# Kernel tuning notes

Hardware: AMD Instinct MI355X
Metric: run time of the kernel (lower is better)

The kernel has to match this reference:

```python
import jax, jax.numpy as jnp
import numpy as np

N_NODES = 100000
N_EDGES = 1600000
F_IN, F_HID, F_OUT = 128, 128, 16
NEG_SLOPE = 0.2


def _glorot(key, shape):
    fan = sum(shape)
    return jax.random.uniform(key, shape, jnp.float32, -1.0, 1.0) * jnp.sqrt(6.0 / fan)


def setup_inputs() -> dict:
    key = jax.random.key(0)
    ks = jax.random.split(key, 16)
    x = jax.random.normal(ks[0], (N_NODES, F_IN), jnp.float32)
    edge_index = jax.random.randint(ks[1], (2, N_EDGES), 0, N_NODES, jnp.int64)
    d1, d2, d3 = F_HID, F_HID // 2, F_OUT
    return {
        'x': x,
        'edge_index': edge_index,
        'W1': _glorot(ks[2], (F_IN, d1)), 'a_src1': _glorot(ks[3], (d1,)), 'a_dst1': _glorot(ks[4], (d1,)), 'b1': jnp.zeros((d1,), jnp.float32),
        'W2': _glorot(ks[5], (d1, d2)), 'a_src2': _glorot(ks[6], (d2,)), 'a_dst2': _glorot(ks[7], (d2,)), 'b2': jnp.zeros((d2,), jnp.float32),
        'W3': _glorot(ks[8], (d2, d3)), 'a_src3': _glorot(ks[9], (d3,)), 'a_dst3': _glorot(ks[10], (d3,)), 'b3': jnp.zeros((d3,), jnp.float32),
    }


def gat_conv(x, src, dst, W, a_s, a_d, b):
    # x: [N, Fin] -> h: [N, Fout]; src/dst: [E] (self-loops included)
    h = x @ W
    e = jax.nn.leaky_relu(h @ a_s, NEG_SLOPE * 0 + NEG_SLOPE)  # placeholder avoided below
    # attention logits per edge: leaky_relu(alpha_src[src] + alpha_dst[dst])
    al_s = h @ a_s  # [N]
    al_d = h @ a_d  # [N]
    logits = jax.nn.leaky_relu(al_s[src] + al_d[dst], NEG_SLOPE)  # [E]
    # numerically stable softmax over incoming edges of each dst node
    m = jax.ops.segment_max(logits, dst, num_segments=N_NODES)
    m = jnp.where(jnp.isfinite(m), m, 0.0)
    ex = jnp.exp(logits - m[dst])
    denom = jax.ops.segment_sum(ex, dst, num_segments=N_NODES)
    alpha = ex / denom[dst]  # self-loops guarantee denom > 0
    out = jax.ops.segment_sum(alpha[:, None] * h[src], dst, num_segments=N_NODES)
    return out + b


def reference(x, edge_index, W1, a_src1, a_dst1, b1, W2, a_src2, a_dst2, b2, W3, a_src3, a_dst3, b3):
    loops = jnp.arange(N_NODES, dtype=edge_index.dtype)
    src = jnp.concatenate([edge_index[0], loops])
    dst = jnp.concatenate([edge_index[1], loops])
    h = gat_conv(x, src, dst, W1, a_src1, a_dst1, b1)
    h = jax.nn.relu(h)  # dropout p=0.5 is identity in eval mode
    h = gat_conv(h, src, dst, W2, a_src2, a_dst2, b2)
    h = jax.nn.relu(h)
    out = gat_conv(h, src, dst, W3, a_src3, a_dst3, b3)
    return out
```

## Files before the change

### kernel.cpp

```cpp
#include <hip/hip_runtime.h>
#include <hip/hip_bf16.h>

typedef __hip_bfloat16 bf16;
typedef __attribute__((ext_vector_type(8))) __bf16 bf16x8;
typedef __attribute__((ext_vector_type(4))) float f32x4;

static constexpr int N = 100000;
static constexpr int E = 1600000;
static constexpr int ETOT = E + N;
static constexpr float SLOPE = 0.2f;

__device__ __constant__ int c_poff[12] = {0, 16384, 16512, 16640,
                                          16768, 24960, 25024, 25088,
                                          25152, 26176, 26192, 26208};
static constexpr int PTOT = 26224;
static constexpr int H_POFF[12] = {0, 16384, 16512, 16640, 16768, 24960,
                                   25024, 25088, 25152, 26176, 26192, 26208};

struct Src12 { const void* p[12]; };

__device__ __forceinline__ float bfLo(unsigned u) { return __uint_as_float(u << 16); }
__device__ __forceinline__ float bfHi(unsigned u) { return __uint_as_float(u & 0xFFFF0000u); }

__device__ __forceinline__ void fma8(const uint4 r, float e, float* acc) {
  acc[0] = fmaf(e, bfLo(r.x), acc[0]);
  acc[1] = fmaf(e, bfHi(r.x), acc[1]);
  acc[2] = fmaf(e, bfLo(r.y), acc[2]);
  acc[3] = fmaf(e, bfHi(r.y), acc[3]);
  acc[4] = fmaf(e, bfLo(r.z), acc[4]);
  acc[5] = fmaf(e, bfHi(r.z), acc[5]);
  acc[6] = fmaf(e, bfLo(r.w), acc[6]);
  acc[7] = fmaf(e, bfHi(r.w), acc[7]);
}

__device__ __forceinline__ float edge_ex(float l) {
  l = (l > 0.f) ? l : SLOPE * l;
  return __expf(l);
}

__device__ __forceinline__ void loadEdge(const int* __restrict__ ei32,
                                         const long long* __restrict__ ei64,
                                         int use64, int t, int& s, int& d) {
  if (t >= E) { s = d = t - E; return; }
  if (use64) { s = (int)ei64[t]; d = (int)ei64[E + t]; }
  else       { s = ei32[t];      d = ei32[E + t]; }
}

static constexpr int NSCAN = (N + 255) / 256;

__global__ __launch_bounds__(256) void detect_zero_kernel(
    const unsigned long long* __restrict__ ei64,
    const unsigned short* __restrict__ w1u16,
    int* __restrict__ flags, int* __restrict__ cnt) {
  const int t = threadIdx.x;
  const int i = blockIdx.x * 256 + t;
  if (i < N) cnt[i] = 0;
  if (blockIdx.x == 0) {
    __shared__ unsigned long long bl[4];
    __shared__ unsigned long long sb64;
    const int w = t >> 6;
    bool p64 = (t < 64) && (ei64[t] >= (unsigned long long)N);
    unsigned long long b64 = __ballot(p64);
    if (t == 0) sb64 = b64;
    bool pf = (((w1u16[t] >> 7) & 0xFFu) >= 126u);
    unsigned long long bf_ = __ballot(pf);
    if ((t & 63) == 0) bl[w] = bf_;
    __syncthreads();
    if (t == 0) {
      flags[0] = (sb64 == 0ull) ? 1 : 0;
      flags[1] = ((bl[0] | bl[1] | bl[2] | bl[3]) != 0ull) ? 1 : 0;
    }
  }
}

static constexpr int PB_DEG = (ETOT + 255) / 256;
static constexpr int PB_X   = N * 128 / 4 / 256;
static constexpr int PB_PAR = (PTOT + 255) / 256;
static constexpr int PB_W1  = 128 * 128 / 256;
static constexpr int PB_W2  = 128 * 64 / 256;
static constexpr int PB_W3  = 64 * 16 / 256;
static constexpr int PB_TOT = PB_DEG + PB_X + PB_PAR + PB_W1 + PB_W2 + PB_W3;

__device__ __forceinline__ void conv_w(const void* W, int kd, int dout, int f32,
                                       bf16* __restrict__ wt, int idx) {
  int n = idx / kd, k = idx - n * kd;
  float v = f32 ? ((const float*)W)[k * dout + n]
                : __bfloat162float(((const bf16*)W)[k * dout + n]);
  wt[idx] = __float2bfloat16(v);
}

__global__ __launch_bounds__(256) void prep_kernel(
    const int* __restrict__ ei32, const long long* __restrict__ ei64,
    const int* __restrict__ flags, int* __restrict__ cnt, int* __restrict__ rank,
    const void* __restrict__ x, bf16* __restrict__ xb,
    Src12 s, float* __restrict__ prm,
    bf16* __restrict__ w1t, bf16* __restrict__ w2t, bf16* __restrict__ w3t) {
  const int b = blockIdx.x, tid = threadIdx.x;
  const int f64 = flags[0], f32 = flags[1];
  if (b < PB_DEG) {
    int t = b * 256 + tid;
    if (t < ETOT) {
      int d = (t >= E) ? (t - E) : (f64 ? (int)ei64[E + t] : ei32[E + t]);
      rank[t] = atomicAdd(&cnt[d], 1);
    }
  } else if (b < PB_DEG + PB_X) {
    int t = (b - PB_DEG) * 256 + tid;
    if (f32) {
      float4 v = ((const float4*)x)[t];
      xb[4 * t + 0] = __float2bfloat16(v.x);
      xb[4 * t + 1] = __float2bfloat16(v.y);
      xb[4 * t + 2] = __float2bfloat16(v.z);
      xb[4 * t + 3] = __float2bfloat16(v.w);
    } else {
      ((uint2*)xb)[t] = ((const uint2*)x)[t];
    }
  } else if (b < PB_DEG + PB_X + PB_PAR) {
    int t = (b - PB_DEG - PB_X) * 256 + tid;
    if (t < PTOT) {
      int k = 0;
#pragma unroll
      for (int i = 1; i < 12; ++i)
        if (t >= c_poff[i]) k = i;
      int j = t - c_poff[k];
      prm[t] = f32 ? ((const float*)s.p[k])[j]
                   : __bfloat162float(((const bf16*)s.p[k])[j]);
    }
  } else if (b < PB_DEG + PB_X + PB_PAR + PB_W1) {
    conv_w(s.p[0], 128, 128, f32, w1t, (b - PB_DEG - PB_X - PB_PAR) * 256 + tid);
  } else if (b < PB_DEG + PB_X + PB_PAR + PB_W1 + PB_W2) {
    conv_w(s.p[4], 128, 64, f32, w2t, (b - PB_DEG - PB_X - PB_PAR - PB_W1) * 256 + tid);
  } else {
    conv_w(s.p[8], 64, 16, f32, w3t, (b - PB_DEG - PB_X - PB_PAR - PB_W1 - PB_W2) * 256 + tid);
  }
}

__global__ __launch_bounds__(256) void scan1_kernel(const int* __restrict__ cnt,
                                                    int* __restrict__ bsum) {
  __shared__ int red[256];
  const int t = threadIdx.x;
  const int i = blockIdx.x * 256 + t;
  red[t] = (i < N) ? cnt[i] : 0;
  __syncthreads();
#pragma unroll
  for (int off = 128; off > 0; off >>= 1) {
    if (t < off) red[t] += red[t + off];
    __syncthreads();
  }
  if (t == 0) bsum[blockIdx.x] = red[0];
}

__global__ __launch_bounds__(1024) void scan2_kernel(const int* __restrict__ bsum,
                                                     int* __restrict__ boff) {
  __shared__ int s[1024];
  const int t = threadIdx.x;
  const int v = (t < NSCAN) ? bsum[t] : 0;
  s[t] = v;
  __syncthreads();
  for (int off = 1; off < 1024; off <<= 1) {
    int u = (t >= off) ? s[t - off] : 0;
    __syncthreads();
    s[t] += u;
    __syncthreads();
  }
  if (t < NSCAN) boff[t] = s[t] - v;
}

__global__ __launch_bounds__(256) void scan3_kernel(const int* __restrict__ cnt,
                                                    const int* __restrict__ boff,
                                                    int* __restrict__ rowptr) {
  __shared__ int s[256];
  const int t = threadIdx.x;
  const int i = blockIdx.x * 256 + t;
  const int v = (i < N) ? cnt[i] : 0;
  s[t] = v;
  __syncthreads();
#pragma unroll
  for (int off = 1; off < 256; off <<= 1) {
    int u = (t >= off) ? s[t - off] : 0;
    __syncthreads();
    s[t] += u;
    __syncthreads();
  }
  if (i < N) rowptr[i] = boff[blockIdx.x] + s[t] - v;
  if (i == 0) rowptr[N] = ETOT;
}

template <int KD, int DOUT>
__device__ __forceinline__ void gemm_body(int bb, const unsigned short* __restrict__ inb,
                                          const unsigned short* __restrict__ wt,
                                          bf16* __restrict__ h,
                                          const float* __restrict__ a_s,
                                          const float* __restrict__ a_d,
                                          float* __restrict__ als,
                                          float* __restrict__ ald) {
  constexpr int SA = KD + 8;
  constexpr int NT = DOUT / 16;
  constexpr int KS = KD / 32;
  __shared__ unsigned short sA[64 * SA];
  __shared__ unsigned short sB[DOUT * SA];
  const int tid = threadIdx.x;
  const int m0 = bb * 64;
  for (int idx = tid; idx < DOUT * KD / 8; idx += 256) {
    int n = idx / (KD / 8), k8 = idx - n * (KD / 8);
    *(uint4*)(sB + n * SA + k8 * 8) = *(const uint4*)(wt + n * KD + k8 * 8);
  }
  for (int idx = tid; idx < 64 * KD / 8; idx += 256) {
    int r = idx / (KD / 8), k8 = idx - r * (KD / 8);
    int m = m0 + r;
    uint4 v = make_uint4(0, 0, 0, 0);
    if (m < N) v = *(const uint4*)(inb + (size_t)m * KD + k8 * 8);
    *(uint4*)(sA + r * SA + k8 * 8) = v;
  }
  __syncthreads();
  const int lane = tid & 63;
  const int wv = tid >> 6;
  const int lr = lane & 15;
  const int q = lane >> 4;
  f32x4 acc[NT];
#pragma unroll
  for (int t = 0; t < NT; ++t)
#pragma unroll
    for (int r = 0; r < 4; ++r) acc[t][r] = 0.f;
  const int arow = wv * 16 + lr;
#pragma unroll
  for (int ks = 0; ks < KS; ++ks) {
    const int k0 = ks * 32 + q * 8;
    const bf16x8 a = *(const bf16x8*)(sA + arow * SA + k0);
#pragma unroll
    for (int t = 0; t < NT; ++t) {
      const bf16x8 b = *(const bf16x8*)(sB + (t * 16 + lr) * SA + k0);
      acc[t] = __builtin_amdgcn_mfma_f32_16x16x32_bf16(a, b, acc[t], 0, 0, 0);
    }
  }
  float ps[4] = {0.f, 0.f, 0.f, 0.f}, pd[4] = {0.f, 0.f, 0.f, 0.f};
#pragma unroll
  for (int t = 0; t < NT; ++t) {
    const float av = a_s[t * 16 + lr];
    const float dv = a_d[t * 16 + lr];
#pragma unroll
    for (int r = 0; r < 4; ++r) {
      ps[r] = fmaf(acc[t][r], av, ps[r]);
      pd[r] = fmaf(acc[t][r], dv, pd[r]);
    }
  }
#pragma unroll
  for (int m = 1; m < 16; m <<= 1)
#pragma unroll
    for (int r = 0; r < 4; ++r) {
      ps[r] += __shfl_xor(ps[r], m, 64);
      pd[r] += __shfl_xor(pd[r], m, 64);
    }
  const int mb = m0 + wv * 16 + q * 4;
  if (lr == 0) {
#pragma unroll
    for (int r = 0; r < 4; ++r) {
      int m = mb + r;
      if (m < N) { als[m] = ps[r]; ald[m] = pd[r]; }
    }
  }
#pragma unroll
  for (int t = 0; t < NT; ++t)
#pragma unroll
    for (int r = 0; r < 4; ++r) {
      int m = mb + r;
      if (m < N) h[(size_t)m * DOUT + t * 16 + lr] = __float2bfloat16(acc[t][r]);
    }
}

template <int KD, int DOUT>
__global__ __launch_bounds__(256) void gemm_al(const unsigned short* __restrict__ inb,
                                               const unsigned short* __restrict__ wt,
                                               bf16* __restrict__ h,
                                               const float* __restrict__ a_s,
                                               const float* __restrict__ a_d,
                                               float* __restrict__ als,
                                               float* __restrict__ ald) {
  gemm_body<KD, DOUT>(blockIdx.x, inb, wt, h, a_s, a_d, als, ald);
}

static constexpr int GB1 = (N + 63) / 64;

__global__ __launch_bounds__(256) void gemm1_scatter(
    const unsigned short* __restrict__ inb, const unsigned short* __restrict__ wt,
    bf16* __restrict__ h, const float* __restrict__ a_s, const float* __restrict__ a_d,
    float* __restrict__ als, float* __restrict__ ald,
    const int* __restrict__ ei32, const long long* __restrict__ ei64,
    const int* __restrict__ flags, const int* __restrict__ rank,
    const int* __restrict__ rowptr, int* __restrict__ ssrt) {
  if (blockIdx.x < GB1) {
    gemm_body<128, 128>(blockIdx.x, inb, wt, h, a_s, a_d, als, ald);
  } else {
    int t = (blockIdx.x - GB1) * 256 + threadIdx.x;
    if (t < ETOT) {
      int s, d;
      loadEdge(ei32, ei64, flags[0], t, s, d);
      ssrt[rowptr[d] + rank[t]] = s;
    }
  }
}

template <int DOUT, bool RELU, bool FINAL>
__global__ __launch_bounds__(256) void aggregate_csr(const int* __restrict__ rowptr,
                                                     const int* __restrict__ ssrt,
                                                     const float* __restrict__ als,
                                                     const float* __restrict__ ald,
                                                     const unsigned short* __restrict__ hb,
                                                     const float* __restrict__ bias,
                                                     bf16* __restrict__ outb,
                                                     void* __restrict__ outv,
                                                     const int* __restrict__ flags) {
  constexpr int TPN = DOUT / 8;
  constexpr int NPB = 256 / TPN;
  const int sub = threadIdx.x % TPN;
  const int d = blockIdx.x * NPB + threadIdx.x / TPN;
  if (d >= N) return;
  const int p0 = rowptr[d], p1 = rowptr[d + 1];
  const float ad = ald[d];
  const int col0 = sub * 8;
  float acc[8];
#pragma unroll
  for (int c = 0; c < 8; ++c) acc[c] = 0.f;
  float sum = 0.f;
  int p = p0;
  for (; p + 4 <= p1; p += 4) {
    const int s0 = ssrt[p + 0];
    const int s1 = ssrt[p + 1];
    const int s2 = ssrt[p + 2];
    const int s3 = ssrt[p + 3];
    const uint4 r0 = *reinterpret_cast<const uint4*>(hb + (size_t)s0 * DOUT + col0);
    const uint4 r1 = *reinterpret_cast<const uint4*>(hb + (size_t)s1 * DOUT + col0);
    const uint4 r2 = *reinterpret_cast<const uint4*>(hb + (size_t)s2 * DOUT + col0);
    const uint4 r3 = *reinterpret_cast<const uint4*>(hb + (size_t)s3 * DOUT + col0);
    const float x0 = edge_ex(als[s0] + ad);
    const float x1 = edge_ex(als[s1] + ad);
    const float x2 = edge_ex(als[s2] + ad);
    const float x3 = edge_ex(als[s3] + ad);
    sum += (x0 + x1) + (x2 + x3);
    fma8(r0, x0, acc);
    fma8(r1, x1, acc);
    fma8(r2, x2, acc);
    fma8(r3, x3, acc);
  }
  for (; p < p1; ++p) {
    const int s = ssrt[p];
    const uint4 r = *reinterpret_cast<const uint4*>(hb + (size_t)s * DOUT + col0);
    const float x = edge_ex(als[s] + ad);
    sum += x;
    fma8(r, x, acc);
  }
  const float inv = 1.f / sum;
  if (FINAL) {
    const bool f32o = flags[1] != 0;
#pragma unroll
    for (int c = 0; c < 8; ++c) {
      float v = acc[c] * inv + bias[col0 + c];
      if (f32o) ((float*)outv)[(size_t)d * DOUT + col0 + c] = v;
      else      ((bf16*)outv)[(size_t)d * DOUT + col0 + c] = __float2bfloat16(v);
    }
  } else {
#pragma unroll
    for (int c = 0; c < 8; ++c) {
      float v = acc[c] * inv + bias[col0 + c];
      if (RELU) v = (v > 0.f) ? v : 0.f;
      outb[(size_t)d * DOUT + col0 + c] = __float2bfloat16(v);
    }
  }
}

static inline size_t rup(size_t v) { return (v + 255) & ~(size_t)255; }

extern "C" void kernel_launch(void* const* d_in, const int* in_sizes, int n_in,
                              void* d_out, int out_size, void* d_ws, size_t ws_size,
                              hipStream_t stream) {
  const int* ei32 = (const int*)d_in[1];
  const long long* ei64 = (const long long*)d_in[1];

  char* p = (char*)d_ws;
  int*   flags  = (int*)p;   p += 256;
  float* prm    = (float*)p; p += rup((size_t)PTOT * 4);
  bf16*  w1t    = (bf16*)p;  p += rup((size_t)128 * 128 * 2);
  bf16*  w2t    = (bf16*)p;  p += rup((size_t)128 * 64 * 2);
  bf16*  w3t    = (bf16*)p;  p += rup((size_t)64 * 16 * 2);
  float* als    = (float*)p; p += rup((size_t)N * 4);
  float* ald    = (float*)p; p += rup((size_t)N * 4);
  int*   rowptr = (int*)p;   p += rup((size_t)(N + 1) * 4);
  int*   cnt    = (int*)p;   p += rup((size_t)N * 4);
  int*   bsum   = (int*)p;   p += rup((size_t)NSCAN * 4);
  int*   boff   = (int*)p;   p += rup((size_t)NSCAN * 4);
  int*   rank   = (int*)p;   p += rup((size_t)ETOT * 4);
  int*   ssrt   = (int*)p;   p += rup((size_t)ETOT * 4);
  bf16*  xb     = (bf16*)p;  p += rup((size_t)N * 128 * 2);
  bf16*  obuf   = (bf16*)p;  p += rup((size_t)N * 128 * 2);
  bf16*  hbuf   = (bf16*)p;

  Src12 s;
  for (int i = 0; i < 12; ++i) s.p[i] = d_in[2 + i];

  detect_zero_kernel<<<NSCAN, 256, 0, stream>>>(
      (const unsigned long long*)d_in[1], (const unsigned short*)d_in[2], flags, cnt);
  prep_kernel<<<PB_TOT, 256, 0, stream>>>(ei32, ei64, flags, cnt, rank,
                                          d_in[0], xb, s, prm, w1t, w2t, w3t);
  scan1_kernel<<<NSCAN, 256, 0, stream>>>(cnt, bsum);
  scan2_kernel<<<1, 1024, 0, stream>>>(bsum, boff);
  scan3_kernel<<<NSCAN, 256, 0, stream>>>(cnt, boff, rowptr);

  const float *as1 = prm + H_POFF[1], *ad1 = prm + H_POFF[2], *b1 = prm + H_POFF[3];
  const float *as2 = prm + H_POFF[5], *ad2 = prm + H_POFF[6], *b2 = prm + H_POFF[7];
  const float *as3 = prm + H_POFF[9], *ad3 = prm + H_POFF[10], *b3 = prm + H_POFF[11];

  gemm1_scatter<<<GB1 + PB_DEG, 256, 0, stream>>>(
      (const unsigned short*)xb, (const unsigned short*)w1t, hbuf, as1, ad1, als, ald,
      ei32, ei64, flags, rank, rowptr, ssrt);
  aggregate_csr<128, true, false><<<(N + 15) / 16, 256, 0, stream>>>(
      rowptr, ssrt, als, ald, (const unsigned short*)hbuf, b1, obuf, nullptr, flags);
  gemm_al<128, 64><<<GB1, 256, 0, stream>>>(
      (const unsigned short*)obuf, (const unsigned short*)w2t, hbuf, as2, ad2, als, ald);
  aggregate_csr<64, true, false><<<(N + 31) / 32, 256, 0, stream>>>(
      rowptr, ssrt, als, ald, (const unsigned short*)hbuf, b2, obuf, nullptr, flags);
  gemm_al<64, 16><<<GB1, 256, 0, stream>>>(
      (const unsigned short*)obuf, (const unsigned short*)w3t, hbuf, as3, ad3, als, ald);
  aggregate_csr<16, false, true><<<(N + 127) / 128, 256, 0, stream>>>(
      rowptr, ssrt, als, ald, (const unsigned short*)hbuf, b3, nullptr, d_out, flags);
}
```

Measured before the change: 379.5 us.

## Build CSR with two-level bucket sort and fuse x conversion into GEMM

Replaces the global-atomic counting sort (one atomic per edge on a per-node counter, then a scatter using rank) with a two-level radix-style bucket sort. Edges are first counted per chunk into 512-node buckets using shared-memory atomics, scanned, scattered into a temporary (dst,src) buffer, and then sorted within each bucket in shared memory to produce rowptr and sorted sources. The separate x-to-bf16 conversion pass is also removed, and the first GEMM now converts fp32 x while loading it. This trades contended global atomics and an extra x round trip for an 8-byte temporary edge buffer and an additional kernel launch. The per-bucket phaseD work is uneven and runs on only about 196 blocks.

```diff
diff --git a/kernel.cpp b/kernel.cpp
--- a/kernel.cpp
+++ b/kernel.cpp
@@ -46,40 +46,43 @@
   else       { s = ei32[t];      d = ei32[E + t]; }
 }
 
-static constexpr int NSCAN = (N + 255) / 256;
-
-__global__ __launch_bounds__(256) void detect_zero_kernel(
+__device__ __forceinline__ unsigned pk2(float a, float b) {
+  bf16 x = __float2bfloat16(a), y = __float2bfloat16(b);
+  unsigned short ux = *(unsigned short*)&x, uy = *(unsigned short*)&y;
+  return ((unsigned)uy << 16) | ux;
+}
+
+static constexpr int CHUNK = 8192;
+static constexpr int NCHK  = (ETOT + CHUNK - 1) / CHUNK;
+static constexpr int NB1   = (N + 511) / 512;
+static constexpr int M1    = NB1 * NCHK;
+static constexpr int SBLK  = (M1 + 255) / 256;
+
+__global__ __launch_bounds__(256) void detect_kernel(
     const unsigned long long* __restrict__ ei64,
-    const unsigned short* __restrict__ w1u16,
-    int* __restrict__ flags, int* __restrict__ cnt) {
+    const unsigned short* __restrict__ w1u16, int* __restrict__ flags) {
   const int t = threadIdx.x;
-  const int i = blockIdx.x * 256 + t;
-  if (i < N) cnt[i] = 0;
-  if (blockIdx.x == 0) {
-    __shared__ unsigned long long bl[4];
-    __shared__ unsigned long long sb64;
-    const int w = t >> 6;
-    bool p64 = (t < 64) && (ei64[t] >= (unsigned long long)N);
-    unsigned long long b64 = __ballot(p64);
-    if (t == 0) sb64 = b64;
-    bool pf = (((w1u16[t] >> 7) & 0xFFu) >= 126u);
-    unsigned long long bf_ = __ballot(pf);
-    if ((t & 63) == 0) bl[w] = bf_;
-    __syncthreads();
-    if (t == 0) {
-      flags[0] = (sb64 == 0ull) ? 1 : 0;
-      flags[1] = ((bl[0] | bl[1] | bl[2] | bl[3]) != 0ull) ? 1 : 0;
-    }
-  }
-}
-
-static constexpr int PB_DEG = (ETOT + 255) / 256;
-static constexpr int PB_X   = N * 128 / 4 / 256;
+  __shared__ unsigned long long bl[4];
+  __shared__ unsigned long long sb64;
+  const int w = t >> 6;
+  bool p64 = (t < 64) && (ei64[t] >= (unsigned long long)N);
+  unsigned long long b64 = __ballot(p64);
+  if (t == 0) sb64 = b64;
+  bool pf = (((w1u16[t] >> 7) & 0xFFu) >= 126u);
+  unsigned long long bf_ = __ballot(pf);
+  if ((t & 63) == 0) bl[w] = bf_;
+  __syncthreads();
+  if (t == 0) {
+    flags[0] = (sb64 == 0ull) ? 1 : 0;
+    flags[1] = ((bl[0] | bl[1] | bl[2] | bl[3]) != 0ull) ? 1 : 0;
+  }
+}
+
 static constexpr int PB_PAR = (PTOT + 255) / 256;
 static constexpr int PB_W1  = 128 * 128 / 256;
 static constexpr int PB_W2  = 128 * 64 / 256;
 static constexpr int PB_W3  = 64 * 16 / 256;
-static constexpr int PB_TOT = PB_DEG + PB_X + PB_PAR + PB_W1 + PB_W2 + PB_W3;
+static constexpr int PB_TOT = NCHK + PB_PAR + PB_W1 + PB_W2 + PB_W3;
 
 __device__ __forceinline__ void conv_w(const void* W, int kd, int dout, int f32,
                                        bf16* __restrict__ wt, int idx) {
@@ -91,31 +94,28 @@
 
 __global__ __launch_bounds__(256) void prep_kernel(
     const int* __restrict__ ei32, const long long* __restrict__ ei64,
-    const int* __restrict__ flags, int* __restrict__ cnt, int* __restrict__ rank,
-    const void* __restrict__ x, bf16* __restrict__ xb,
+    const int* __restrict__ flags, int* __restrict__ c1,
     Src12 s, float* __restrict__ prm,
     bf16* __restrict__ w1t, bf16* __restrict__ w2t, bf16* __restrict__ w3t) {
   const int b = blockIdx.x, tid = threadIdx.x;
   const int f64 = flags[0], f32 = flags[1];
-  if (b < PB_DEG) {
-    int t = b * 256 + tid;
-    if (t < ETOT) {
-      int d = (t >= E) ? (t - E) : (f64 ? (int)ei64[E + t] : ei32[E + t]);
-      rank[t] = atomicAdd(&cnt[d], 1);
-    }
-  } else if (b < PB_DEG + PB_X) {
-    int t = (b - PB_DEG) * 256 + tid;
-    if (f32) {
-      float4 v = ((const float4*)x)[t];
-      xb[4 * t + 0] = __float2bfloat16(v.x);
-      xb[4 * t + 1] = __float2bfloat16(v.y);
-      xb[4 * t + 2] = __float2bfloat16(v.z);
-      xb[4 * t + 3] = __float2bfloat16(v.w);
-    } else {
-      ((uint2*)xb)[t] = ((const uint2*)x)[t];
-    }
-  } else if (b < PB_DEG + PB_X + PB_PAR) {
-    int t = (b - PB_DEG - PB_X) * 256 + tid;
+  if (b < NCHK) {
+    __shared__ int h1[NB1];
+    if (tid < NB1) h1[tid] = 0;
+    __syncthreads();
+    const int t0 = b * CHUNK;
+#pragma unroll 4
+    for (int i = tid; i < CHUNK; i += 256) {
+      int t = t0 + i;
+      if (t < ETOT) {
+        int d = (t >= E) ? (t - E) : (f64 ? (int)ei64[E + t] : ei32[E + t]);
+        atomicAdd(&h1[d >> 9], 1);
+      }
+    }
+    __syncthreads();
+    if (tid < NB1) c1[tid * NCHK + b] = h1[tid];
+  } else if (b < NCHK + PB_PAR) {
+    int t = (b - NCHK) * 256 + tid;
     if (t < PTOT) {
       int k = 0;
 #pragma unroll
@@ -125,21 +125,21 @@
       prm[t] = f32 ? ((const float*)s.p[k])[j]
                    : __bfloat162float(((const bf16*)s.p[k])[j]);
     }
-  } else if (b < PB_DEG + PB_X + PB_PAR + PB_W1) {
-    conv_w(s.p[0], 128, 128, f32, w1t, (b - PB_DEG - PB_X - PB_PAR) * 256 + tid);
-  } else if (b < PB_DEG + PB_X + PB_PAR + PB_W1 + PB_W2) {
-    conv_w(s.p[4], 128, 64, f32, w2t, (b - PB_DEG - PB_X - PB_PAR - PB_W1) * 256 + tid);
+  } else if (b < NCHK + PB_PAR + PB_W1) {
+    conv_w(s.p[0], 128, 128, f32, w1t, (b - NCHK - PB_PAR) * 256 + tid);
+  } else if (b < NCHK + PB_PAR + PB_W1 + PB_W2) {
+    conv_w(s.p[4], 128, 64, f32, w2t, (b - NCHK - PB_PAR - PB_W1) * 256 + tid);
   } else {
-    conv_w(s.p[8], 64, 16, f32, w3t, (b - PB_DEG - PB_X - PB_PAR - PB_W1 - PB_W2) * 256 + tid);
-  }
-}
-
-__global__ __launch_bounds__(256) void scan1_kernel(const int* __restrict__ cnt,
+    conv_w(s.p[8], 64, 16, f32, w3t, (b - NCHK - PB_PAR - PB_W1 - PB_W2) * 256 + tid);
+  }
+}
+
+__global__ __launch_bounds__(256) void scanA_kernel(const int* __restrict__ c1,
                                                     int* __restrict__ bsum) {
   __shared__ int red[256];
   const int t = threadIdx.x;
   const int i = blockIdx.x * 256 + t;
-  red[t] = (i < N) ? cnt[i] : 0;
+  red[t] = (i < M1) ? c1[i] : 0;
   __syncthreads();
 #pragma unroll
   for (int off = 128; off > 0; off >>= 1) {
@@ -149,29 +149,29 @@
   if (t == 0) bsum[blockIdx.x] = red[0];
 }
 
-__global__ __launch_bounds__(1024) void scan2_kernel(const int* __restrict__ bsum,
-                                                     int* __restrict__ boff) {
-  __shared__ int s[1024];
+__global__ __launch_bounds__(256) void scanB_kernel(const int* __restrict__ bsum,
+                                                    int* __restrict__ boff) {
+  __shared__ int s[256];
   const int t = threadIdx.x;
-  const int v = (t < NSCAN) ? bsum[t] : 0;
+  const int v = (t < SBLK) ? bsum[t] : 0;
   s[t] = v;
   __syncthreads();
-  for (int off = 1; off < 1024; off <<= 1) {
+  for (int off = 1; off < 256; off <<= 1) {
     int u = (t >= off) ? s[t - off] : 0;
     __syncthreads();
     s[t] += u;
     __syncthreads();
   }
-  if (t < NSCAN) boff[t] = s[t] - v;
-}
-
-__global__ __launch_bounds__(256) void scan3_kernel(const int* __restrict__ cnt,
+  if (t < SBLK) boff[t] = s[t] - v;
+}
+
+__global__ __launch_bounds__(256) void scanC_kernel(const int* __restrict__ c1,
                                                     const int* __restrict__ boff,
-                                                    int* __restrict__ rowptr) {
+                                                    int* __restrict__ off1) {
   __shared__ int s[256];
   const int t = threadIdx.x;
   const int i = blockIdx.x * 256 + t;
-  const int v = (i < N) ? cnt[i] : 0;
+  const int v = (i < M1) ? c1[i] : 0;
   s[t] = v;
   __syncthreads();
 #pragma unroll
@@ -181,12 +181,77 @@
     s[t] += u;
     __syncthreads();
   }
-  if (i < N) rowptr[i] = boff[blockIdx.x] + s[t] - v;
-  if (i == 0) rowptr[N] = ETOT;
-}
-
-template <int KD, int DOUT>
-__device__ __forceinline__ void gemm_body(int bb, const unsigned short* __restrict__ inb,
+  if (i < M1) off1[i] = boff[blockIdx.x] + s[t] - v;
+}
+
+__device__ __forceinline__ void phaseC_body(int c, const int* __restrict__ ei32,
+                                            const long long* __restrict__ ei64,
+                                            int f64, const int* __restrict__ off1,
+                                            int2* __restrict__ tmp) {
+  __shared__ int cur[NB1];
+  const int tid = threadIdx.x;
+  if (tid < NB1) cur[tid] = off1[tid * NCHK + c];
+  __syncthreads();
+  const int t0 = c * CHUNK;
+#pragma unroll 4
+  for (int i = tid; i < CHUNK; i += 256) {
+    int t = t0 + i;
+    if (t < ETOT) {
+      int s, d;
+      loadEdge(ei32, ei64, f64, t, s, d);
+      int pos = atomicAdd(&cur[d >> 9], 1);
+      tmp[pos] = make_int2(d, s);
+    }
+  }
+}
+
+__global__ __launch_bounds__(256) void phaseD_kernel(const int* __restrict__ off1,
+                                                     const int2* __restrict__ tmp,
+                                                     int* __restrict__ rowptr,
+                                                     int* __restrict__ ssrt) {
+  __shared__ int h2[512], e2[512], cur[512];
+  __shared__ int ps[256];
+  const int b = blockIdx.x, t = threadIdx.x;
+  const int base = off1[b * NCHK];
+  const int end = (b + 1 < NB1) ? off1[(b + 1) * NCHK] : ETOT;
+  const int len = end - base;
+  h2[2 * t] = 0; h2[2 * t + 1] = 0;
+  __syncthreads();
+  for (int i = t; i < len; i += 256)
+    atomicAdd(&h2[tmp[base + i].x & 511], 1);
+  __syncthreads();
+  const int s1 = h2[2 * t], s2 = h2[2 * t + 1];
+  ps[t] = s1 + s2;
+  __syncthreads();
+  for (int off = 1; off < 256; off <<= 1) {
+    int u = (t >= off) ? ps[t - off] : 0;
+    __syncthreads();
+    ps[t] += u;
+    __syncthreads();
+  }
+  const int ep = ps[t] - (s1 + s2);
+  e2[2 * t] = ep;
+  e2[2 * t + 1] = ep + s1;
+  cur[2 * t] = ep;
+  cur[2 * t + 1] = ep + s1;
+  __syncthreads();
+#pragma unroll
+  for (int k = 0; k < 2; ++k) {
+    int f = 2 * t + k;
+    int node = (b << 9) + f;
+    if (node < N) rowptr[node] = base + e2[f];
+  }
+  if (b == 0 && t == 0) rowptr[N] = ETOT;
+  for (int i = t; i < len; i += 256) {
+    int2 e = tmp[base + i];
+    int pos = base + atomicAdd(&cur[e.x & 511], 1);
+    ssrt[pos] = e.y;
+  }
+}
+
+template <int KD, int DOUT, bool XD>
+__device__ __forceinline__ void gemm_body(int bb, const void* __restrict__ inv,
+                                          const int* __restrict__ flags,
                                           const unsigned short* __restrict__ wt,
                                           bf16* __restrict__ h,
                                           const float* __restrict__ a_s,
@@ -204,11 +269,21 @@
     int n = idx / (KD / 8), k8 = idx - n * (KD / 8);
     *(uint4*)(sB + n * SA + k8 * 8) = *(const uint4*)(wt + n * KD + k8 * 8);
   }
+  const bool f32 = XD ? (flags[1] != 0) : false;
   for (int idx = tid; idx < 64 * KD / 8; idx += 256) {
     int r = idx / (KD / 8), k8 = idx - r * (KD / 8);
     int m = m0 + r;
     uint4 v = make_uint4(0, 0, 0, 0);
-    if (m < N) v = *(const uint4*)(inb + (size_t)m * KD + k8 * 8);
+    if (m < N) {
+      if (XD && f32) {
+        const float4 v0 = *((const float4*)inv + ((size_t)m * KD + k8 * 8) / 4);
+        const float4 v1 = *((const float4*)inv + ((size_t)m * KD + k8 * 8) / 4 + 1);
+        v = make_uint4(pk2(v0.x, v0.y), pk2(v0.z, v0.w),
+                       pk2(v1.x, v1.y), pk2(v1.z, v1.w));
+      } else {
+        v = *((const uint4*)inv + ((size_t)m * KD + k8 * 8) / 8);
+      }
+    }
     *(uint4*)(sA + r * SA + k8 * 8) = v;
   }
   __syncthreads();
@@ -275,27 +350,23 @@
                                                const float* __restrict__ a_d,
                                                float* __restrict__ als,
                                                float* __restrict__ ald) {
-  gemm_body<KD, DOUT>(blockIdx.x, inb, wt, h, a_s, a_d, als, ald);
+  gemm_body<KD, DOUT, false>(blockIdx.x, inb, nullptr, wt, h, a_s, a_d, als, ald);
 }
 
 static constexpr int GB1 = (N + 63) / 64;
 
-__global__ __launch_bounds__(256) void gemm1_scatter(
-    const unsigned short* __restrict__ inb, const unsigned short* __restrict__ wt,
-    bf16* __restrict__ h, const float* __restrict__ a_s, const float* __restrict__ a_d,
+__global__ __launch_bounds__(256) void gemm1_phaseC(
+    const void* __restrict__ x, const int* __restrict__ flags,
+    const unsigned short* __restrict__ wt, bf16* __restrict__ h,
+    const float* __restrict__ a_s, const float* __restrict__ a_d,
     float* __restrict__ als, float* __restrict__ ald,
     const int* __restrict__ ei32, const long long* __restrict__ ei64,
-    const int* __restrict__ flags, const int* __restrict__ rank,
-    const int* __restrict__ rowptr, int* __restrict__ ssrt) {
+    const int* __restrict__ off1, int2* __restrict__ tmp) {
   if (blockIdx.x < GB1) {
-    gemm_body<128, 128>(blockIdx.x, inb, wt, h, a_s, a_d, als, ald);
+    gemm_body<128, 128, true>(blockIdx.x, x, flags, wt, h, a_s, a_d, als, ald);
   } else {
-    int t = (blockIdx.x - GB1) * 256 + threadIdx.x;
-    if (t < ETOT) {
-      int s, d;
-      loadEdge(ei32, ei64, flags[0], t, s, d);
-      ssrt[rowptr[d] + rank[t]] = s;
-    }
+    int c = blockIdx.x - GB1;
+    if (c < NCHK) phaseC_body(c, ei32, ei64, flags[0], off1, tmp);
   }
 }
 
@@ -384,33 +455,33 @@
   float* als    = (float*)p; p += rup((size_t)N * 4);
   float* ald    = (float*)p; p += rup((size_t)N * 4);
   int*   rowptr = (int*)p;   p += rup((size_t)(N + 1) * 4);
-  int*   cnt    = (int*)p;   p += rup((size_t)N * 4);
-  int*   bsum   = (int*)p;   p += rup((size_t)NSCAN * 4);
-  int*   boff   = (int*)p;   p += rup((size_t)NSCAN * 4);
-  int*   rank   = (int*)p;   p += rup((size_t)ETOT * 4);
+  int*   c1     = (int*)p;   p += rup((size_t)M1 * 4);
+  int*   off1   = (int*)p;   p += rup((size_t)M1 * 4);
+  int*   bsum   = (int*)p;   p += rup((size_t)SBLK * 4);
+  int*   boff   = (int*)p;   p += rup((size_t)SBLK * 4);
+  int2*  tmp    = (int2*)p;  p += rup((size_t)ETOT * 8);
   int*   ssrt   = (int*)p;   p += rup((size_t)ETOT * 4);
-  bf16*  xb     = (bf16*)p;  p += rup((size_t)N * 128 * 2);
   bf16*  obuf   = (bf16*)p;  p += rup((size_t)N * 128 * 2);
   bf16*  hbuf   = (bf16*)p;
 
   Src12 s;
   for (int i = 0; i < 12; ++i) s.p[i] = d_in[2 + i];
 
-  detect_zero_kernel<<<NSCAN, 256, 0, stream>>>(
-      (const unsigned long long*)d_in[1], (const unsigned short*)d_in[2], flags, cnt);
-  prep_kernel<<<PB_TOT, 256, 0, stream>>>(ei32, ei64, flags, cnt, rank,
-                                          d_in[0], xb, s, prm, w1t, w2t, w3t);
-  scan1_kernel<<<NSCAN, 256, 0, stream>>>(cnt, bsum);
-  scan2_kernel<<<1, 1024, 0, stream>>>(bsum, boff);
-  scan3_kernel<<<NSCAN, 256, 0, stream>>>(cnt, boff, rowptr);
+  detect_kernel<<<1, 256, 0, stream>>>(
+      (const unsigned long long*)d_in[1], (const unsigned short*)d_in[2], flags);
+  prep_kernel<<<PB_TOT, 256, 0, stream>>>(ei32, ei64, flags, c1, s, prm, w1t, w2t, w3t);
+  scanA_kernel<<<SBLK, 256, 0, stream>>>(c1, bsum);
+  scanB_kernel<<<1, 256, 0, stream>>>(bsum, boff);
+  scanC_kernel<<<SBLK, 256, 0, stream>>>(c1, boff, off1);
 
   const float *as1 = prm + H_POFF[1], *ad1 = prm + H_POFF[2], *b1 = prm + H_POFF[3];
   const float *as2 = prm + H_POFF[5], *ad2 = prm + H_POFF[6], *b2 = prm + H_POFF[7];
   const float *as3 = prm + H_POFF[9], *ad3 = prm + H_POFF[10], *b3 = prm + H_POFF[11];
 
-  gemm1_scatter<<<GB1 + PB_DEG, 256, 0, stream>>>(
-      (const unsigned short*)xb, (const unsigned short*)w1t, hbuf, as1, ad1, als, ald,
-      ei32, ei64, flags, rank, rowptr, ssrt);
+  gemm1_phaseC<<<GB1 + NCHK, 256, 0, stream>>>(
+      d_in[0], flags, (const unsigned short*)w1t, hbuf, as1, ad1, als, ald,
+      ei32, ei64, off1, tmp);
+  phaseD_kernel<<<NB1, 256, 0, stream>>>(off1, tmp, rowptr, ssrt);
   aggregate_csr<128, true, false><<<(N + 15) / 16, 256, 0, stream>>>(
       rowptr, ssrt, als, ald, (const unsigned short*)hbuf, b1, obuf, nullptr, flags);
   gemm_al<128, 64><<<GB1, 256, 0, stream>>>(
```

Result: faster. 336.8 us (-11.2%).
